# Kernel tuning notes

Measured on AMD Instinct MI355X. Metric: run time of the kernel, lower is better.

## Reference

```python
import jax, jax.numpy as jnp
import numpy as np

SQRT2 = float(np.sqrt(2.0))
DIST_KERNEL = jnp.asarray([SQRT2, 1.0, SQRT2, SQRT2, 1.0, SQRT2], dtype=jnp.float32)
LAMBDA_WI = 0.5


def setup_inputs() -> dict:
    key = jax.random.key(0)
    x = jax.random.normal(key, (32, 1, 64, 2048), dtype=jnp.float32)
    return {"x": x}


def _new_pixels(x):
    # Equivalent of F.unfold(x, kernel_size=(2,3), padding=(0,1), stride=(1,1)):
    # windows over (H-1) x W output positions, 6 taps each, in row-major tap order.
    B, C, H, W = x.shape
    xp = jnp.pad(x, ((0, 0), (0, 0), (0, 0), (1, 1)))  # pad width only
    # [B, C, H-1, W, 6]
    w = jnp.stack(
        [xp[:, :, i : i + H - 1, j : j + W] for i in (0, 1) for j in (0, 1, 2)],
        axis=-1,
    )
    nonzero = (w != 0).astype(w.dtype)
    gmin = jnp.min(w)  # torch.min(kernel) is a GLOBAL min over the whole windows tensor
    wi = jnp.exp(-LAMBDA_WI * DIST_KERNEL) * (2.0 / (1.0 + jnp.exp(w - gmin))) * nonzero
    num = jnp.sum(w * wi, axis=-1)   # [B, C, H-1, W]
    den = jnp.sum(wi, axis=-1)
    den = jnp.where(den == 0, 1.0, den)
    return num / den


def reference(x):
    B, C, H, W = x.shape
    pixels = _new_pixels(x)  # [B, C, H-1, W]
    # Interleave original rows (even) with interpolated rows (odd), then the torch
    # code's dstack drops the trailing zero row and appends the last input row,
    # yielding ... x[H-2], p[H-2], x[H-1], x[H-1]  -> total 2H rows.
    interleaved = jnp.stack([x[:, :, :-1, :], pixels], axis=3).reshape(B, C, 2 * (H - 1), W)
    last = x[:, :, -1:, :]
    return jnp.concatenate([interleaved, last, last], axis=2)  # [B, C, 2H, W]
```

## Files before the change

### kernel.cpp

```cpp
#include <hip/hip_runtime.h>
#include <stdint.h>

#define BB   32
#define HH   64
#define WW   2048
#define HOUT 128
#define NB1  1024
#define NT   256

typedef float f4 __attribute__((ext_vector_type(4)));

__global__ void __launch_bounds__(NT)
k1_min_copy(const float* __restrict__ x, float* __restrict__ out,
            float* __restrict__ partial) {
    const int tid = threadIdx.x;
    const f4* x4 = (const f4*)x;
    float m = 3.4e38f;

    int i = blockIdx.x * NT + tid;
    #pragma unroll
    for (int it = 0; it < (BB * HH * WW / 4) / (NB1 * NT); ++it, i += NB1 * NT) {
        f4 v = x4[i];
        m = fminf(fminf(v.x, v.y), fminf(fminf(v.z, v.w), m));

        int b   = i >> 15;
        int rem = i & 32767;
        int h   = rem >> 9;
        int wq  = rem & 511;

        f4* o = (f4*)(out + ((size_t)(b * HOUT) + 2 * h) * WW) + wq;
        __builtin_nontemporal_store(v, o);
        if (h == 63) {
            f4* o2 = (f4*)(out + ((size_t)(b * HOUT) + 127) * WW) + wq;
            __builtin_nontemporal_store(v, o2);
        }
    }

    #pragma unroll
    for (int off = 32; off > 0; off >>= 1)
        m = fminf(m, __shfl_down(m, off, 64));
    __shared__ float smem[4];
    if ((tid & 63) == 0) smem[tid >> 6] = m;
    __syncthreads();
    if (tid == 0)
        partial[blockIdx.x] =
            fminf(fminf(smem[0], smem[1]), fminf(smem[2], smem[3]));
}

__global__ void __launch_bounds__(NT)
k2_pixels(const float* __restrict__ x, float* __restrict__ out,
          const float* __restrict__ partial) {
    __shared__ float smem[4];
    const int tid = threadIdx.x;

    float p = fminf(fminf(partial[tid], partial[tid + 256]),
                    fminf(partial[tid + 512], partial[tid + 768]));
    #pragma unroll
    for (int off = 32; off > 0; off >>= 1)
        p = fminf(p, __shfl_down(p, off, 64));
    if ((tid & 63) == 0) smem[tid >> 6] = p;
    __syncthreads();
    const float gmin = fminf(
        fminf(fminf(smem[0], smem[1]), fminf(smem[2], smem[3])), 0.0f);

    int blk = blockIdx.x;
    int b   = blk / 126;
    int r   = blk - b * 126;
    int h   = r >> 1;
    int w0  = ((r & 1) << 10) + (tid << 2);

    const float* rA = x + ((size_t)(b * HH) + h) * WW + w0;
    const float* rB = rA + WW;

    f4 a  = *(const f4*)rA;
    f4 c4 = *(const f4*)rB;
    float aL = (w0 > 0)      ? rA[-1] : 0.0f;
    float bL = (w0 > 0)      ? rB[-1] : 0.0f;
    float aR = (w0 + 4 < WW) ? rA[4]  : 0.0f;
    float bR = (w0 + 4 < WW) ? rB[4]  : 0.0f;

    float av[6] = {aL, a.x, a.y, a.z, a.w, aR};
    float bv[6] = {bL, c4.x, c4.y, c4.z, c4.w, bR};

    const float BASE_D = 0.49306869139523979f;
    const float BASE_C = 0.60653065971263342f;

    f4 res;
    #pragma unroll
    for (int c = 0; c < 4; ++c) {
        float num = 0.0f, den = 0.0f;
        float vs[6] = {av[c], av[c + 1], av[c + 2],
                       bv[c], bv[c + 1], bv[c + 2]};
        const float bs[6] = {BASE_D, BASE_C, BASE_D, BASE_D, BASE_C, BASE_D};
        #pragma unroll
        for (int k = 0; k < 6; ++k) {
            float wv = vs[k];
            float e  = __expf(wv - gmin);
            float wi = bs[k] * 2.0f * __builtin_amdgcn_rcpf(1.0f + e);
            wi = (wv != 0.0f) ? wi : 0.0f;
            num += wv * wi;
            den += wi;
        }
        den = (den == 0.0f) ? 1.0f : den;
        res[c] = num * __builtin_amdgcn_rcpf(den);
    }

    f4* o = (f4*)(out + ((size_t)(b * HOUT) + 2 * h + 1) * WW + w0);
    __builtin_nontemporal_store(res, o);
}

extern "C" void kernel_launch(void* const* d_in, const int* in_sizes, int n_in,
                              void* d_out, int out_size, void* d_ws, size_t ws_size,
                              hipStream_t stream) {
    const float* x = (const float*)d_in[0];
    float* out = (float*)d_out;
    float* partial = (float*)d_ws;

    hipLaunchKernelGGL(k1_min_copy, dim3(NB1), dim3(NT), 0, stream,
                       x, out, partial);
    hipLaunchKernelGGL(k2_pixels, dim3(BB * 63 * 2), dim3(NT), 0, stream,
                       x, out, partial);
}
```

Measured before the change: 21.68 us.

## Move row copies into second kernel and make first kernel a pure min reduction

The first kernel now only computes the global-min partials (with twice as many blocks). All output writing moves to the second kernel, which covers every output row: even rows and the final row are copied straight from x, odd rows are interpolated. Block indices are swizzled by XCD (bid&7) to spread work. This shortens the first kernel's write traffic so the min reduction finishes sooner. The cost is that x is read twice, and the second kernel's partial reduction now spans 2048 entries.

```diff
diff --git a/kernel.cpp b/kernel.cpp
--- a/kernel.cpp
+++ b/kernel.cpp
@@ -5,37 +5,22 @@
 #define HH   64
 #define WW   2048
 #define HOUT 128
-#define NB1  1024
+#define NB1  2048
 #define NT   256
 
 typedef float f4 __attribute__((ext_vector_type(4)));
 
 __global__ void __launch_bounds__(NT)
-k1_min_copy(const float* __restrict__ x, float* __restrict__ out,
-            float* __restrict__ partial) {
+k1_min(const float* __restrict__ x, float* __restrict__ partial) {
     const int tid = threadIdx.x;
     const f4* x4 = (const f4*)x;
     float m = 3.4e38f;
-
     int i = blockIdx.x * NT + tid;
     #pragma unroll
     for (int it = 0; it < (BB * HH * WW / 4) / (NB1 * NT); ++it, i += NB1 * NT) {
         f4 v = x4[i];
         m = fminf(fminf(v.x, v.y), fminf(fminf(v.z, v.w), m));
-
-        int b   = i >> 15;
-        int rem = i & 32767;
-        int h   = rem >> 9;
-        int wq  = rem & 511;
-
-        f4* o = (f4*)(out + ((size_t)(b * HOUT) + 2 * h) * WW) + wq;
-        __builtin_nontemporal_store(v, o);
-        if (h == 63) {
-            f4* o2 = (f4*)(out + ((size_t)(b * HOUT) + 127) * WW) + wq;
-            __builtin_nontemporal_store(v, o2);
-        }
     }
-
     #pragma unroll
     for (int off = 32; off > 0; off >>= 1)
         m = fminf(m, __shfl_down(m, off, 64));
@@ -48,13 +33,31 @@
 }
 
 __global__ void __launch_bounds__(NT)
-k2_pixels(const float* __restrict__ x, float* __restrict__ out,
-          const float* __restrict__ partial) {
-    __shared__ float smem[4];
+k2_all(const float* __restrict__ x, float* __restrict__ out,
+       const float* __restrict__ partial) {
     const int tid = threadIdx.x;
 
-    float p = fminf(fminf(partial[tid], partial[tid + 256]),
-                    fminf(partial[tid + 512], partial[tid + 768]));
+    int bid  = blockIdx.x;
+    int work = (bid & 7) * 1024 + (bid >> 3);
+    int b    = work >> 8;
+    int rem  = work & 255;
+    int ho   = rem >> 1;
+    int w0   = ((rem & 1) << 10) + (tid << 2);
+
+    float* orow = out + ((size_t)(b * HOUT) + ho) * WW + w0;
+    int h = ho >> 1;
+
+    if ((ho & 1) == 0 || ho == 127) {
+        f4 v = *(const f4*)(x + ((size_t)(b * HH) + h) * WW + w0);
+        __builtin_nontemporal_store(v, (f4*)orow);
+        return;
+    }
+
+    __shared__ float smem[4];
+    float p = 3.4e38f;
+    #pragma unroll
+    for (int k = 0; k < NB1 / NT; ++k)
+        p = fminf(p, partial[tid + k * NT]);
     #pragma unroll
     for (int off = 32; off > 0; off >>= 1)
         p = fminf(p, __shfl_down(p, off, 64));
@@ -62,12 +65,6 @@
     __syncthreads();
     const float gmin = fminf(
         fminf(fminf(smem[0], smem[1]), fminf(smem[2], smem[3])), 0.0f);
-
-    int blk = blockIdx.x;
-    int b   = blk / 126;
-    int r   = blk - b * 126;
-    int h   = r >> 1;
-    int w0  = ((r & 1) << 10) + (tid << 2);
 
     const float* rA = x + ((size_t)(b * HH) + h) * WW + w0;
     const float* rB = rA + WW;
@@ -105,8 +102,7 @@
         res[c] = num * __builtin_amdgcn_rcpf(den);
     }
 
-    f4* o = (f4*)(out + ((size_t)(b * HOUT) + 2 * h + 1) * WW + w0);
-    __builtin_nontemporal_store(res, o);
+    __builtin_nontemporal_store(res, (f4*)orow);
 }
 
 extern "C" void kernel_launch(void* const* d_in, const int* in_sizes, int n_in,
@@ -116,8 +112,7 @@
     float* out = (float*)d_out;
     float* partial = (float*)d_ws;
 
-    hipLaunchKernelGGL(k1_min_copy, dim3(NB1), dim3(NT), 0, stream,
-                       x, out, partial);
-    hipLaunchKernelGGL(k2_pixels, dim3(BB * 63 * 2), dim3(NT), 0, stream,
+    hipLaunchKernelGGL(k1_min, dim3(NB1), dim3(NT), 0, stream, x, partial);
+    hipLaunchKernelGGL(k2_all, dim3(BB * HOUT * 2), dim3(NT), 0, stream,
                        x, out, partial);
 }
```

After: 25.90 us. 19.5% more time.
